# Performance work log

Measured on AMD Instinct MI355X. Metric: run time of the kernel, lower is better.

The kernel has to match this reference:

```python
import jax, jax.numpy as jnp
import numpy as np

B, H, W = 16, 16, 16
DIM = 768
NH = 8
HD = DIM // NH
NEXP = 8
TOPK = 2
DSTATE = 1
DTRANK = 4
KDIR = 4


def setup_inputs() -> dict:
    key = jax.random.key(0)
    ks = jax.random.split(key, 16)
    s = 1.0 / float(np.sqrt(DIM))
    inp = {
        'x': jax.random.normal(ks[0], (B, H, W, DIM)),
        'sa_in_w': jax.random.normal(ks[1], (3 * DIM, DIM)) * s,
        'sa_in_b': jnp.zeros((3 * DIM,)),
        'sa_out_w': jax.random.normal(ks[2], (DIM, DIM)) * s,
        'sa_out_b': jnp.zeros((DIM,)),
        'ca_in_w': jax.random.normal(ks[3], (2 * DIM, DIM)) * s,
        'ca_in_b': jnp.zeros((2 * DIM,)),
        'expert_queries': jax.random.normal(ks[4], (NEXP, DIM)) * s,
        'e_in_w': jax.random.normal(ks[5], (NEXP, 2 * DIM, DIM)) * s,
        'e_in_b': jnp.zeros((NEXP, 2 * DIM)),
        'e_conv_w': jax.random.normal(ks[6], (NEXP, DIM, 1, 3, 3)) / 3.0,
        'e_conv_b': jnp.zeros((NEXP, DIM)),
        'e_xproj_w': jax.random.normal(ks[7], (NEXP, KDIR, DTRANK + 2 * DSTATE, DIM)) * s,
        'e_dtproj_w': jax.random.normal(ks[8], (NEXP, KDIR, DIM, DTRANK)) * 0.1,
        'e_dtproj_b': jax.random.uniform(ks[9], (NEXP, KDIR, DIM), minval=-4.0, maxval=-2.0),
        'e_Alog': jax.random.uniform(ks[10], (NEXP, KDIR, DIM, DSTATE), minval=0.0, maxval=1.0),
        'e_D': jnp.ones((NEXP, KDIR, DIM)),
        'e_ln_scale': jnp.ones((NEXP, DIM)),
        'e_ln_bias': jnp.zeros((NEXP, DIM)),
    }
    return {k: v.astype(jnp.float32) for k, v in inp.items()}


def _selective_scan(xs, Wx, Wdt, bdt, Alog, D):
    # xs: [B, L, d]; Wx: [R+2N, d]; Wdt: [d, R]; Alog: [d, N]; D: [d]
    dbl = jnp.einsum('bld,ed->ble', xs, Wx)
    dt = jax.nn.softplus(jnp.einsum('blr,dr->bld', dbl[..., :DTRANK], Wdt) + bdt)
    Bm = dbl[..., DTRANK:DTRANK + DSTATE]
    Cm = dbl[..., DTRANK + DSTATE:]
    A = -jnp.exp(Alog)  # [d, N]

    def step(h, t):
        dt_t, B_t, C_t, x_t = t  # [b,d],[b,N],[b,N],[b,d]
        h = jnp.exp(dt_t[:, :, None] * A) * h + (dt_t * x_t)[:, :, None] * B_t[:, None, :]
        return h, jnp.einsum('bdn,bn->bd', h, C_t)

    b, L, d = xs.shape
    h0 = jnp.zeros((b, d, DSTATE), xs.dtype)
    tm = lambda a: jnp.moveaxis(a, 1, 0)
    _, ys = jax.lax.scan(step, h0, (tm(dt), tm(Bm), tm(Cm), tm(xs)))
    return jnp.moveaxis(ys, 0, 1) + D * xs


def _expert(in_w, in_b, conv_w, conv_b, xproj_w, dtp_w, dtp_b, Alog, D, ln_s, ln_b, x):
    b = x.shape[0]
    xz = jnp.einsum('bhwc,oc->bhwo', x, in_w) + in_b
    xc, z = jnp.split(xz, 2, axis=-1)
    xn = jax.lax.conv_general_dilated(jnp.transpose(xc, (0, 3, 1, 2)), conv_w,
                                      (1, 1), ((1, 1), (1, 1)), feature_group_count=DIM)
    xc = jax.nn.silu(jnp.transpose(xn + conv_b[None, :, None, None], (0, 2, 3, 1)))
    L = H * W
    xh = xc.reshape(b, L, DIM)                              # row-major 'h'
    xv = jnp.transpose(xc, (0, 2, 1, 3)).reshape(b, L, DIM)  # col-major 'v'
    seqs = jnp.stack([xh, xh[:, ::-1], xv, xv[:, ::-1]])     # [4, b, L, d]
    ys = jax.vmap(_selective_scan)(seqs, xproj_w, dtp_w, dtp_b, Alog, D)
    yv = ys[2] + ys[3][:, ::-1]
    yv = jnp.transpose(yv.reshape(b, W, H, DIM), (0, 2, 1, 3)).reshape(b, L, DIM)
    y = (ys[0] + ys[1][:, ::-1] + yv).reshape(b, H, W, DIM)
    mu = y.mean(-1, keepdims=True)
    var = ((y - mu) ** 2).mean(-1, keepdims=True)
    y = (y - mu) * jax.lax.rsqrt(var + 1e-5) * ln_s + ln_b   # out_norm (LayerNorm)
    y = y * jax.nn.silu(z)
    return y.mean((1, 2))  # AdaptiveAvgPool2d((1,1)) -> [b, DIM]


def _forward(x, sa_in_w, sa_in_b, sa_out_w, sa_out_b, ca_in_w, ca_in_b, expert_queries,
             e_in_w, e_in_b, e_conv_w, e_conv_b, e_xproj_w, e_dtproj_w, e_dtproj_b,
             e_Alog, e_D, e_ln_scale, e_ln_bias):
    b = x.shape[0]
    L = H * W
    scale = 1.0 / float(np.sqrt(HD))
    xs = x.reshape(b, L, DIM)
    # spatial self-attention (eval mode: dropout off)
    qkv = xs @ sa_in_w.T + sa_in_b
    q, k, v = [a.reshape(b, L, NH, HD) for a in jnp.split(qkv, 3, -1)]
    att = jax.nn.softmax(jnp.einsum('bqhd,bkhd->bhqk', q, k) * scale, -1)
    ctx = jnp.einsum('bhqk,bkhd->bqhd', att, v).reshape(b, L, DIM) @ sa_out_w.T + sa_out_b
    # expert cross-attention: only head-averaged attention weights are used
    q2 = (ctx @ ca_in_w[:DIM].T + ca_in_b[:DIM]).reshape(b, L, NH, HD)
    k2 = (expert_queries @ ca_in_w[DIM:].T + ca_in_b[DIM:]).reshape(NEXP, NH, HD)
    aw = jax.nn.softmax(jnp.einsum('blhd,ehd->bhle', q2, k2) * scale, -1).mean(1)  # [b,L,E]
    gate = jax.nn.softmax(aw.mean(1), -1)  # [b, E]
    tk_scores, tk_idx = jax.lax.top_k(gate, TOPK)
    wgt = jax.nn.softmax(tk_scores, -1)
    # dense expert compute (all experts on all samples), then gather top-k
    all_out = jax.vmap(_expert, in_axes=(0,) * 11 + (None,))(
        e_in_w, e_in_b, e_conv_w, e_conv_b, e_xproj_w, e_dtproj_w, e_dtproj_b,
        e_Alog, e_D, e_ln_scale, e_ln_bias, x)  # [E, b, DIM]
    per_b = jnp.transpose(all_out, (1, 0, 2))  # [b, E, DIM]
    sel = jnp.take_along_axis(per_b, tk_idx[:, :, None], axis=1)  # [b, K, DIM]
    return jnp.sum(wgt[:, :, None] * sel, axis=1)  # [b, DIM]


def reference(x, sa_in_w, sa_in_b, sa_out_w, sa_out_b, ca_in_w, ca_in_b, expert_queries,
              e_in_w, e_in_b, e_conv_w, e_conv_b, e_xproj_w, e_dtproj_w, e_dtproj_b,
              e_Alog, e_D, e_ln_scale, e_ln_bias):
    return _forward(x, sa_in_w, sa_in_b, sa_out_w, sa_out_b, ca_in_w, ca_in_b, expert_queries,
                    e_in_w, e_in_b, e_conv_w, e_conv_b, e_xproj_w, e_dtproj_w, e_dtproj_b,
                    e_Alog, e_D, e_ln_scale, e_ln_bias)
```

## Files before the change

kernel.cpp:

```cpp
#include <hip/hip_runtime.h>
#include <hip/hip_bf16.h>


#define LTOK 256
#define DIMC 768

typedef unsigned short ushortt;
typedef __attribute__((ext_vector_type(8))) short bf16x8;
typedef __attribute__((ext_vector_type(4))) float f32x4;

#define LOG2E 1.44269504f
#define LN2   0.69314718f

__device__ __forceinline__ float fexp2(float x) { return __builtin_amdgcn_exp2f(x); }
__device__ __forceinline__ float flog2(float x) { return __builtin_amdgcn_logf(x); }

__device__ __forceinline__ ushortt f2b(float f) {
  union { float f; unsigned u; } c; c.f = f;
  unsigned r = (c.u + 0x7FFFu + ((c.u >> 16) & 1u)) >> 16;
  return (ushortt)r;
}

__global__ __launch_bounds__(256) void mk_mcast4(
    const float* __restrict__ s0, ushortt* __restrict__ d0,
    const float* __restrict__ s1, ushortt* __restrict__ d1,
    const float* __restrict__ s2, ushortt* __restrict__ d2,
    const float* __restrict__ s3, ushortt* __restrict__ d3)
{
  long g = (long)blockIdx.x * 256 + threadIdx.x;
  const float* s; ushortt* dst; long o;
  if (g < 786432)       { s = s0; dst = d0; o = g; }
  else if (g < 1228800) { s = s1; dst = d1; o = g - 786432; }
  else if (g < 1376256) { s = s2; dst = d2; o = g - 1228800; }
  else                  { s = s3; dst = d3; o = g - 1376256; }
  o <<= 2;
  float4 v = *(const float4*)(s + o);
  ushort4 w;
  w.x = f2b(v.x); w.y = f2b(v.y); w.z = f2b(v.z); w.w = f2b(v.w);
  *(ushort4*)(dst + o) = w;
}

__global__ __launch_bounds__(256) void mk_cast(const float* __restrict__ in,
                                               ushortt* __restrict__ outp, long n)
{
  long i = ((long)blockIdx.x * 256 + threadIdx.x) * 4;
  if (i + 3 < n) {
    float4 v = *(const float4*)(in + i);
    ushort4 o;
    o.x = f2b(v.x); o.y = f2b(v.y); o.z = f2b(v.z); o.w = f2b(v.w);
    *(ushort4*)(outp + i) = o;
  }
}

__global__ __launch_bounds__(256) void mk_mfma(
    const ushortt* __restrict__ A, const ushortt* __restrict__ B,
    const float* __restrict__ bias, void* __restrict__ C,
    int K, int lda, int ldb, int ldc,
    int zdiv, long sA1, long sA2, long sB1, long sB2, long sC1, long sC2,
    long sBias,
    const int* __restrict__ pairExp, int tilesN,
    int outBf, int splitN, void* __restrict__ C2, int ldc2, int outBf2, int c2vt)
{
  int z = blockIdx.y;
  long aoff, boff, coff, biasoff = 0;
  if (pairExp) {
    int e = pairExp[z];
    aoff = (long)(z >> 1) * sA1; boff = (long)e * sB1;
    coff = (long)z * sC1; biasoff = (long)e * sBias;
  } else {
    int z1 = z / zdiv, z2 = z - z1 * zdiv;
    aoff = (long)z1 * sA1 + (long)z2 * sA2;
    boff = (long)z1 * sB1 + (long)z2 * sB2;
    coff = (long)z1 * sC1 + (long)z2 * sC2;
  }
  int tile = blockIdx.x;
  int tm = tile / tilesN, tn = tile - tm * tilesN;
  long m0 = (long)tm << 7, n0 = (long)tn << 7;

  __shared__ ushortt As[128][40];
  __shared__ ushortt Bs[128][40];

  int tid = threadIdx.x;
  int lane = tid & 63, wvi = tid >> 6;
  int wr = wvi >> 1, wc = wvi & 1;
  int lm = lane & 15, lg = lane >> 4;

  f32x4 zero4 = {0.f, 0.f, 0.f, 0.f};
  f32x4 acc[4][4];
#pragma unroll
  for (int i = 0; i < 4; i++)
#pragma unroll
    for (int j = 0; j < 4; j++) acc[i][j] = zero4;

  const ushortt* Ab = A + aoff;
  const ushortt* Bb = B + boff;

  for (int k0 = 0; k0 < K; k0 += 32) {
#pragma unroll
    for (int h = 0; h < 2; h++) {
      int q = tid + h * 256;
      int row = q >> 2, ck = (q & 3) << 3;
      *(uint4*)&As[row][ck] = *(const uint4*)(Ab + (m0 + row) * lda + k0 + ck);
      *(uint4*)&Bs[row][ck] = *(const uint4*)(Bb + (n0 + row) * ldb + k0 + ck);
    }
    __syncthreads();
    bf16x8 af[4], bfr[4];
#pragma unroll
    for (int i = 0; i < 4; i++)
      af[i] = *(const bf16x8*)&As[wr * 64 + i * 16 + lm][lg << 3];
#pragma unroll
    for (int j = 0; j < 4; j++)
      bfr[j] = *(const bf16x8*)&Bs[wc * 64 + j * 16 + lm][lg << 3];
#pragma unroll
    for (int i = 0; i < 4; i++)
#pragma unroll
      for (int j = 0; j < 4; j++)
        acc[i][j] = __builtin_amdgcn_mfma_f32_16x16x32_bf16(af[i], bfr[j], acc[i][j], 0, 0, 0);
    __syncthreads();
  }

#pragma unroll
  for (int mt = 0; mt < 4; mt++) {
#pragma unroll
    for (int nt = 0; nt < 4; nt++) {
      long grow = m0 + wr * 64 + mt * 16 + lg * 4;
      long gcol = n0 + wc * 64 + nt * 16 + lm;
      float bv = bias ? bias[biasoff + gcol] : 0.f;
      if ((int)gcol < splitN) {
#pragma unroll
        for (int r = 0; r < 4; r++) {
          float v = acc[mt][nt][r] + bv;
          long idx = coff + (grow + r) * ldc + gcol;
          if (outBf) ((ushortt*)C)[idx] = f2b(v);
          else ((float*)C)[idx] = v;
        }
      } else if (c2vt) {
        int cc = (int)gcol - splitN;
        int hh = cc / 96, jj = cc - hh * 96;
#pragma unroll
        for (int r = 0; r < 4; r++) {
          float v = acc[mt][nt][r] + bv;
          long gr = grow + r;
          long b = gr >> 8, t = gr & 255;
          long idx = (((b * 8 + hh) * 128 + jj) << 8) + t;
          ((ushortt*)C2)[idx] = f2b(v);
        }
      } else {
        long col = gcol - splitN;
#pragma unroll
        for (int r = 0; r < 4; r++) {
          float v = acc[mt][nt][r] + bv;
          long idx = coff + (grow + r) * ldc2 + col;
          if (outBf2) ((ushortt*)C2)[idx] = f2b(v);
          else ((float*)C2)[idx] = v;
        }
      }
    }
  }
}

__global__ __launch_bounds__(256) void mk_gemm(
    const float* __restrict__ A, const float* __restrict__ B,
    const float* __restrict__ bias, float* __restrict__ C,
    int M, int N, int K, int lda, int ldb, int ldc, int tilesN)
{
  int tile = blockIdx.x;
  int tm = tile / tilesN, tn = tile - tm * tilesN;
  int m0 = tm << 6, n0 = tn << 6;

  __shared__ float As[16][68];
  __shared__ float Bs[16][68];

  int tid = threadIdx.x;
  int tx = tid & 15, ty = tid >> 4;
  int lrow = tid >> 2;
  int lk = (tid & 3) << 2;

  float acc[4][4];
#pragma unroll
  for (int i = 0; i < 4; i++)
#pragma unroll
    for (int j = 0; j < 4; j++) acc[i][j] = 0.f;

  for (int k0 = 0; k0 < K; k0 += 16) {
    {
      int gm = m0 + lrow;
      float4 v = {0.f, 0.f, 0.f, 0.f};
      if (gm < M) v = *(const float4*)(A + (long)gm * lda + (k0 + lk));
      As[lk + 0][lrow] = v.x; As[lk + 1][lrow] = v.y;
      As[lk + 2][lrow] = v.z; As[lk + 3][lrow] = v.w;
    }
    {
      int gn = n0 + lrow;
      float4 v = {0.f, 0.f, 0.f, 0.f};
      if (gn < N) v = *(const float4*)(B + (long)gn * ldb + (k0 + lk));
      Bs[lk + 0][lrow] = v.x; Bs[lk + 1][lrow] = v.y;
      Bs[lk + 2][lrow] = v.z; Bs[lk + 3][lrow] = v.w;
    }
    __syncthreads();
#pragma unroll
    for (int kk = 0; kk < 16; kk++) {
      float4 a = *(const float4*)&As[kk][ty << 2];
      float4 b = *(const float4*)&Bs[kk][tx << 2];
      acc[0][0] += a.x * b.x; acc[0][1] += a.x * b.y; acc[0][2] += a.x * b.z; acc[0][3] += a.x * b.w;
      acc[1][0] += a.y * b.x; acc[1][1] += a.y * b.y; acc[1][2] += a.y * b.z; acc[1][3] += a.y * b.w;
      acc[2][0] += a.z * b.x; acc[2][1] += a.z * b.y; acc[2][2] += a.z * b.z; acc[2][3] += a.z * b.w;
      acc[3][0] += a.w * b.x; acc[3][1] += a.w * b.y; acc[3][2] += a.w * b.z; acc[3][3] += a.w * b.w;
    }
    __syncthreads();
  }

#pragma unroll
  for (int i = 0; i < 4; i++) {
    int gm = m0 + (ty << 2) + i;
    if (gm >= M) continue;
#pragma unroll
    for (int j = 0; j < 4; j++) {
      int gn = n0 + (tx << 2) + j;
      if (gn >= N) continue;
      float v = acc[i][j];
      if (bias) v += bias[gn];
      C[(long)gm * ldc + gn] = v;
    }
  }
}

__global__ __launch_bounds__(256) void mk_softmax(const float* __restrict__ scores,
                                                  ushortt* __restrict__ att, float scale)
{
  int row = (blockIdx.x << 2) + (threadIdx.x >> 6);
  int lane = threadIdx.x & 63;
  const float* p = scores + (long)row * 256 + (lane << 2);
  float4 v = *(const float4*)p;
  float m = fmaxf(fmaxf(v.x, v.y), fmaxf(v.z, v.w));
#pragma unroll
  for (int o = 32; o; o >>= 1) m = fmaxf(m, __shfl_xor(m, o, 64));
  float sl = scale * LOG2E;
  v.x = fexp2(sl * (v.x - m));
  v.y = fexp2(sl * (v.y - m));
  v.z = fexp2(sl * (v.z - m));
  v.w = fexp2(sl * (v.w - m));
  float s = v.x + v.y + v.z + v.w;
#pragma unroll
  for (int o = 32; o; o >>= 1) s += __shfl_xor(s, o, 64);
  float r = 1.f / s;
  ushort4 o4;
  o4.x = f2b(v.x * r); o4.y = f2b(v.y * r); o4.z = f2b(v.z * r); o4.w = f2b(v.w * r);
  *(ushort4*)(att + (long)row * 256 + (lane << 2)) = o4;
}

__global__ __launch_bounds__(256) void mk_gates(const float* __restrict__ q2,
                                                const float* __restrict__ k2,
                                                float* __restrict__ gacc)
{
  __shared__ float k2p[8 * 808];
  int b = blockIdx.x >> 4, q = blockIdx.x & 15;
  for (int i = threadIdx.x; i < 6144; i += 256) {
    int e = i / 768, rem = i - e * 768;
    int h = rem / 96, j = rem - h * 96;
    k2p[e * 808 + h * 100 + j] = k2[i];
  }
  __syncthreads();
  const float scale = 0.10206207261596577f;
  int wid = threadIdx.x >> 6, lane = threadIdx.x & 63;
  int h = lane >> 3, e = lane & 7;
  const float* kp = &k2p[e * 808 + h * 100];
  float accL = 0.f;
#pragma unroll
  for (int ti = 0; ti < 4; ti++) {
    int l = q * 16 + wid * 4 + ti;
    const float* qh = q2 + ((long)b * LTOK + l) * DIMC + h * 96;
    float sum = 0.f;
#pragma unroll
    for (int j = 0; j < 96; j += 4) {
      float4 qv = *(const float4*)(qh + j);
      float4 kv = *(const float4*)(kp + j);
      sum += qv.x * kv.x + qv.y * kv.y + qv.z * kv.z + qv.w * kv.w;
    }
    float s = sum * scale;
    float mx = s;
#pragma unroll
    for (int o = 1; o <= 4; o <<= 1) mx = fmaxf(mx, __shfl_xor(mx, o, 64));
    float ex = fexp2((s - mx) * LOG2E);
    float se = ex;
#pragma unroll
    for (int o = 1; o <= 4; o <<= 1) se += __shfl_xor(se, o, 64);
    accL += ex / se;
  }
#pragma unroll
  for (int o = 8; o <= 32; o <<= 1) accL += __shfl_xor(accL, o, 64);
  __shared__ float red[4][8];
  if (lane < 8) red[wid][lane] = accL;
  __syncthreads();
  if (threadIdx.x < 8) {
    float v = red[0][threadIdx.x] + red[1][threadIdx.x] +
              red[2][threadIdx.x] + red[3][threadIdx.x];
    atomicAdd(&gacc[b * 8 + threadIdx.x], v);
  }
}

__global__ __launch_bounds__(64) void mk_gatetop(const float* __restrict__ gacc,
                                                 int* __restrict__ pe,
                                                 float* __restrict__ pw)
{
  int b = threadIdx.x;
  if (b >= 16) return;
  float g[8];
  for (int e = 0; e < 8; e++) g[e] = gacc[b * 8 + e] * (1.f / (8.f * 256.f));
  float mx = g[0];
  for (int e = 1; e < 8; e++) mx = fmaxf(mx, g[e]);
  float se = 0.f;
  for (int e = 0; e < 8; e++) { g[e] = expf(g[e] - mx); se += g[e]; }
  for (int e = 0; e < 8; e++) g[e] /= se;
  int i0 = 0;
  for (int e = 1; e < 8; e++) if (g[e] > g[i0]) i0 = e;
  int i1 = (i0 == 0) ? 1 : 0;
  for (int e = 0; e < 8; e++) if (e != i0 && g[e] > g[i1]) i1 = e;
  float w0 = 1.f / (1.f + expf(g[i1] - g[i0]));
  pe[2 * b] = i0; pe[2 * b + 1] = i1;
  pw[2 * b] = w0; pw[2 * b + 1] = 1.f - w0;
}

__global__ __launch_bounds__(768) void mk_conv(const float* __restrict__ xzx,
                                               const float* __restrict__ cw,
                                               const float* __restrict__ cb,
                                               const int* __restrict__ pe,
                                               float* __restrict__ xc)
{
  int blk = blockIdx.x;
  int p = blk >> 8, t = blk & 255;
  int e = pe[p];
  int h = t >> 4, w = t & 15;
  int c = threadIdx.x;
  const float* wp = cw + ((long)e * DIMC + c) * 9;
  float acc = cb[e * DIMC + c];
#pragma unroll
  for (int dh = 0; dh < 3; dh++) {
    int hh = h + dh - 1;
    if (hh < 0 || hh > 15) continue;
#pragma unroll
    for (int dw = 0; dw < 3; dw++) {
      int ww = w + dw - 1;
      if (ww < 0 || ww > 15) continue;
      acc += xzx[((long)p * LTOK + hh * 16 + ww) * DIMC + c] * wp[dh * 3 + dw];
    }
  }
  xc[((long)p * LTOK + t) * DIMC + c] = acc / (1.f + fexp2(-acc * LOG2E));
}

__device__ __forceinline__ int tmap(int dir, int s) {
  if (dir == 0) return s;
  if (dir == 1) return 255 - s;
  if (dir == 2) return ((s & 15) << 4) | (s >> 4);
  int u = 255 - s;
  return ((u & 15) << 4) | (u >> 4);
}

__global__ __launch_bounds__(256) void mk_dbl(const float* __restrict__ xc,
                                              const float* __restrict__ xproj,
                                              const int* __restrict__ pe,
                                              float* __restrict__ dblm)
{
  int p = blockIdx.x >> 6;
  int tq = blockIdx.x & 63;
  int wid = threadIdx.x >> 6, lane = threadIdx.x & 63;
  int m = tq * 4 + wid;
  int e = pe[p];
  const float* xr = xc + ((long)p * LTOK + m) * DIMC;
  const float* wb = xproj + (long)e * 24 * DIMC;
  float4 xv[3];
#pragma unroll
  for (int j = 0; j < 3; j++) xv[j] = *(const float4*)(xr + j * 256 + lane * 4);
  float acc[24];
#pragma unroll
  for (int r = 0; r < 24; r++) {
    const float* wr = wb + r * DIMC;
    float s = 0.f;
#pragma unroll
    for (int j = 0; j < 3; j++) {
      float4 wv = *(const float4*)(wr + j * 256 + lane * 4);
      s += xv[j].x * wv.x + xv[j].y * wv.y + xv[j].z * wv.z + xv[j].w * wv.w;
    }
    acc[r] = s;
  }
#pragma unroll
  for (int r = 0; r < 24; r++)
#pragma unroll
    for (int o = 32; o; o >>= 1) acc[r] += __shfl_xor(acc[r], o, 64);
  if (lane == 0) {
    float* o = dblm + ((long)p * LTOK + m) * 24;
#pragma unroll
    for (int r = 0; r < 24; r++) o[r] = acc[r];
  }
}

__global__ __launch_bounds__(512) void mk_scan(const float* __restrict__ xc,
                                               const float* __restrict__ dblm,
                                               const float* __restrict__ dtw,
                                               const float* __restrict__ dtb,
                                               const float* __restrict__ Alog,
                                               const float* __restrict__ Dp,
                                               const int* __restrict__ pe,
                                               float* __restrict__ yac)
{
  __shared__ float dbS[256 * 24];
  __shared__ float yS[256 * 17];
  __shared__ float aS[32][16];
  __shared__ float hS[32][16];
  __shared__ float dsum[16];
  int blk = blockIdx.x;
  int p = blk / 48, cg = blk - p * 48;
  int c0 = cg << 4;
  int e = pe[p];
  int tid = threadIdx.x;
  {
    const float4* src = (const float4*)(dblm + (long)p * LTOK * 24);
    float4* dst = (float4*)dbS;
    for (int i = tid; i < 1536; i += 512) dst[i] = src[i];
  }
  for (int i = tid; i < 256 * 17; i += 512) yS[i] = 0.f;
  if (tid < 16) {
    float s = 0.f;
#pragma unroll
    for (int dd = 0; dd < 4; dd++) s += Dp[(long)(e * 4 + dd) * DIMC + c0 + tid];
    dsum[tid] = s;
  }
  __syncthreads();

  int c = tid & 15;
  int rr = tid >> 4;
  int seg = rr & 7;
  int dir = rr >> 3;
  int d = c0 + c;
  const float* xcp = xc + (long)p * LTOK * DIMC;
  long pb = (long)(e * 4 + dir) * DIMC + d;
  float4 wv = *(const float4*)(dtw + pb * 4);
  float bdt = dtb[pb];
  float Ad = -fexp2(Alog[pb] * LOG2E);
  int t0 = seg << 5;

  float h = 0.f, ap = 1.f;
  for (int tb = 0; tb < 32; tb += 8) {
    float xv[8]; int mm[8];
#pragma unroll
    for (int i = 0; i < 8; i++) {
      mm[i] = tmap(dir, t0 + tb + i);
      xv[i] = xcp[(long)mm[i] * DIMC + d];
    }
#pragma unroll
    for (int i = 0; i < 8; i++) {
      const float* db = &dbS[mm[i] * 24 + dir * 6];
      float xr = wv.x * db[0] + wv.y * db[1] + wv.z * db[2] + wv.w * db[3] + bdt;
      float te = fexp2(xr * LOG2E);
      float g = flog2(1.f + te);
      g = (xr > 60.f) ? xr * LOG2E : g;
      float de = fexp2(g * Ad);
      h = de * h + (g * LN2) * xv[i] * db[4];
      ap *= de;
    }
  }
  aS[rr][c] = ap;
  hS[rr][c] = h;
  __syncthreads();

  float hh = 0.f;
  for (int j = dir * 8; j < rr; j++)
    hh = aS[j][c] * hh + hS[j][c];

  for (int tb = 0; tb < 32; tb += 8) {
    float xv[8]; int mm[8];
#pragma unroll
    for (int i = 0; i < 8; i++) {
      mm[i] = tmap(dir, t0 + tb + i);
      xv[i] = xcp[(long)mm[i] * DIMC + d];
    }
#pragma unroll
    for (int i = 0; i < 8; i++) {
      const float* db = &dbS[mm[i] * 24 + dir * 6];
      float xr = wv.x * db[0] + wv.y * db[1] + wv.z * db[2] + wv.w * db[3] + bdt;
      float te = fexp2(xr * LOG2E);
      float g = flog2(1.f + te);
      g = (xr > 60.f) ? xr * LOG2E : g;
      float de = fexp2(g * Ad);
      hh = de * hh + (g * LN2) * xv[i] * db[4];
      atomicAdd(&yS[mm[i] * 17 + c], hh * db[5]);
    }
  }
  __syncthreads();

  float* yp = yac + (long)p * LTOK * DIMC + c0;
  for (int i = tid; i < 256 * 16; i += 512) {
    int t = i >> 4, cz = i & 15;
    yp[(long)t * DIMC + cz] = yS[t * 17 + cz] + xcp[(long)t * DIMC + c0 + cz] * dsum[cz];
  }
}

__global__ __launch_bounds__(256) void mk_lnfin(const float* __restrict__ yac,
                                                const float* __restrict__ xzz,
                                                const float* __restrict__ lns,
                                                const float* __restrict__ lnb,
                                                const int* __restrict__ pe,
                                                float* __restrict__ eo)
{
  int blk = blockIdx.x;
  int p = blk >> 4, ts = blk & 15;
  int e = pe[p];
  int tid = threadIdx.x;
  int wid = tid >> 6, lane = tid & 63;
  float ls[12], lb[12], acc[12];
#pragma unroll
  for (int i = 0; i < 12; i++) {
    int d = i * 64 + lane;
    ls[i] = lns[e * DIMC + d];
    lb[i] = lnb[e * DIMC + d];
    acc[i] = 0.f;
  }
#pragma unroll
  for (int tt = 0; tt < 4; tt++) {
    int t = ts * 16 + wid * 4 + tt;
    const float* yr = yac + ((long)p * LTOK + t) * DIMC;
    const float* zr = xzz + ((long)p * LTOK + t) * DIMC;
    float v[12];
    float s = 0.f;
#pragma unroll
    for (int i = 0; i < 12; i++) { v[i] = yr[i * 64 + lane]; s += v[i]; }
#pragma unroll
    for (int o = 32; o; o >>= 1) s += __shfl_xor(s, o, 64);
    float mu = s * (1.f / 768.f);
    float sq = 0.f;
#pragma unroll
    for (int i = 0; i < 12; i++) { float dlt = v[i] - mu; sq += dlt * dlt; }
#pragma unroll
    for (int o = 32; o; o >>= 1) sq += __shfl_xor(sq, o, 64);
    float rs = rsqrtf(sq * (1.f / 768.f) + 1e-5f);
#pragma unroll
    for (int i = 0; i < 12; i++) {
      float y = (v[i] - mu) * rs * ls[i] + lb[i];
      float z = zr[i * 64 + lane];
      y *= z / (1.f + fexp2(-z * LOG2E));
      acc[i] += y;
    }
  }
  __shared__ float sacc[768];
  for (int j = tid; j < 768; j += 256) sacc[j] = 0.f;
  __syncthreads();
#pragma unroll
  for (int i = 0; i < 12; i++) atomicAdd(&sacc[i * 64 + lane], acc[i]);
  __syncthreads();
  for (int j = tid; j < 768; j += 256) atomicAdd(&eo[(long)p * DIMC + j], sacc[j]);
}

__global__ __launch_bounds__(768) void mk_out(const float* __restrict__ eo,
                                              const float* __restrict__ pw,
                                              float* __restrict__ out)
{
  int b = blockIdx.x, d = threadIdx.x;
  float v = pw[2 * b] * eo[(long)(2 * b) * DIMC + d] +
            pw[2 * b + 1] * eo[(long)(2 * b + 1) * DIMC + d];
  out[b * DIMC + d] = v * (1.f / 256.f);
}

extern "C" void kernel_launch(void* const* d_in, const int* in_sizes, int n_in,
                              void* d_out, int out_size, void* d_ws, size_t ws_size,
                              hipStream_t stream)
{
  const float* x        = (const float*)d_in[0];
  const float* sa_in_w  = (const float*)d_in[1];
  const float* sa_in_b  = (const float*)d_in[2];
  const float* sa_out_w = (const float*)d_in[3];
  const float* sa_out_b = (const float*)d_in[4];
  const float* ca_in_w  = (const float*)d_in[5];
  const float* ca_in_b  = (const float*)d_in[6];
  const float* eq       = (const float*)d_in[7];
  const float* e_in_w   = (const float*)d_in[8];
  const float* e_in_b   = (const float*)d_in[9];
  const float* e_conv_w = (const float*)d_in[10];
  const float* e_conv_b = (const float*)d_in[11];
  const float* e_xproj  = (const float*)d_in[12];
  const float* e_dtw    = (const float*)d_in[13];
  const float* e_dtb    = (const float*)d_in[14];
  const float* e_Alog   = (const float*)d_in[15];
  const float* e_D      = (const float*)d_in[16];
  const float* e_lns    = (const float*)d_in[17];
  const float* e_lnb    = (const float*)d_in[18];
  float* out = (float*)d_out;

  float* ws = (float*)d_ws;
  ushortt* qk_b   = (ushortt*)(ws + 0);
  float*   scores = ws + 6291456;
  ushortt* dump_b = (ushortt*)(ws + 6291456);
  ushortt* ctxa_b = (ushortt*)(ws + 7864320);
  ushortt* att_b  = (ushortt*)(ws + 14680064);
  ushortt* vt_b   = (ushortt*)(ws + 18874368);
  ushortt* xb     = (ushortt*)(ws + 20971520);
  ushortt* wqkv_b = (ushortt*)(ws + 22544384);
  ushortt* saow_b = (ushortt*)(ws + 23429120);
  ushortt* caw_b  = (ushortt*)(ws + 23724032);
  ushortt* ctx_b  = (ushortt*)(ws + 0);
  float*   q2     = ws + 1572864;
  float*   k2     = ws + 25165824;
  int*     pe     = (int*)(ws + 25171968);
  float*   pw     = ws + 25172000;
  float*   eo     = ws + 25172032;
  float*   dblm   = ws + 25196608;
  float*   gacc   = ws + 25393216;
  float*   xz_x   = ws + 0;
  float*   xz_z   = ws + 6291456;
  ushortt* ew_b   = (ushortt*)(ws + 12582912);
  float*   xc     = ws + 12582912;
  float*   yac    = ws + 18874368;

  const float scale = 0.10206207261596577f;

  mk_mcast4<<<5952, 256, 0, stream>>>(x, xb, sa_in_w, wqkv_b, sa_out_w, saow_b,
                                      ca_in_w, caw_b);
  mk_mfma<<<dim3(576, 1), 256, 0, stream>>>(xb, wqkv_b, sa_in_b, qk_b,
      768, 768, 768, 1536, 1, 0, 0, 0, 0, 0, 0, 0, nullptr, 18,
      1, 1536, vt_b, 0, 1, 1);
  mk_mfma<<<dim3(4, 128), 256, 0, stream>>>(qk_b, qk_b + 768, nullptr, scores,
      96, 1536, 1536, 256, 8, 393216, 96, 393216, 96, 524288, 65536, 0, nullptr, 2,
      0, 1 << 30, nullptr, 0, 0, 0);
  mk_softmax<<<8192, 256, 0, stream>>>(scores, att_b, scale);
  mk_mfma<<<dim3(2, 128), 256, 0, stream>>>(att_b, vt_b, nullptr, ctxa_b,
      256, 256, 256, 768, 8, 524288, 65536, 262144, 32768, 196608, 96, 0, nullptr, 1,
      1, 96, dump_b, 32, 1, 0);
  mk_cast<<<9216, 256, 0, stream>>>(e_in_w, ew_b, 9437184);
  mk_mfma<<<dim3(192, 1), 256, 0, stream>>>(ctxa_b, saow_b, sa_out_b, ctx_b,
      768, 768, 768, 768, 1, 0, 0, 0, 0, 0, 0, 0, nullptr, 6,
      1, 1 << 30, nullptr, 0, 0, 0);
  mk_mfma<<<dim3(192, 1), 256, 0, stream>>>(ctx_b, caw_b, ca_in_b, q2,
      768, 768, 768, 768, 1, 0, 0, 0, 0, 0, 0, 0, nullptr, 6,
      0, 1 << 30, nullptr, 0, 0, 0);
  mk_gemm<<<dim3(12, 1), 256, 0, stream>>>(eq, ca_in_w + 589824, ca_in_b + 768, k2,
      8, 768, 768, 768, 768, 768, 12);
  (void)hipMemsetAsync(gacc, 0, 128 * sizeof(float), stream);
  (void)hipMemsetAsync(eo, 0, 24576 * sizeof(float), stream);
  mk_gates<<<256, 256, 0, stream>>>(q2, k2, gacc);
  mk_gatetop<<<1, 64, 0, stream>>>(gacc, pe, pw);
  mk_mfma<<<dim3(24, 32), 256, 0, stream>>>(xb, ew_b, e_in_b, xz_x,
      768, 768, 768, 768, 1, 196608, 0, 1179648, 0, 196608, 0, 1536, pe, 12,
      0, 768, xz_z, 768, 0, 0);
  mk_conv<<<32 * 256, 768, 0, stream>>>(xz_x, e_conv_w, e_conv_b, pe, xc);
  mk_dbl<<<2048, 256, 0, stream>>>(xc, e_xproj, pe, dblm);
  mk_scan<<<1536, 512, 0, stream>>>(xc, dblm, e_dtw, e_dtb, e_Alog, e_D, pe, yac);
  mk_lnfin<<<512, 256, 0, stream>>>(yac, xz_z, e_lns, e_lnb, pe, eo);
  mk_out<<<16, 768, 0, stream>>>(eo, pw, out);

  (void)in_sizes; (void)n_in; (void)out_size; (void)ws_size;
}
```

Baseline: 635.0 us.

## Stage scan inputs in LDS with swizzled layouts and cache first-pass decay terms

The selective-scan kernel now copies its xc tile into shared memory once, with a padded and swizzled layout, instead of reading global memory in both scan passes. The dblm buffer is padded to 32 floats per token so the dt/B/C values can be fetched as float4 loads with a bank-rotating swizzle. The first pass keeps per-step decay and increment values in registers so the second pass skips recomputing the exp/log softplus. The change also adds an occupancy hint to launch bounds and moves dblm to workspace offset 0, which raises register pressure and risks spills or aliasing with live buffers.

```diff
diff --git a/kernel.cpp b/kernel.cpp
--- a/kernel.cpp
+++ b/kernel.cpp
@@ -388,13 +388,13 @@
 #pragma unroll
     for (int o = 32; o; o >>= 1) acc[r] += __shfl_xor(acc[r], o, 64);
   if (lane == 0) {
-    float* o = dblm + ((long)p * LTOK + m) * 24;
-#pragma unroll
-    for (int r = 0; r < 24; r++) o[r] = acc[r];
-  }
-}
-
-__global__ __launch_bounds__(512) void mk_scan(const float* __restrict__ xc,
+    float* o = dblm + ((long)p * LTOK + m) * 32;
+#pragma unroll
+    for (int r = 0; r < 24; r++) o[(r / 6) * 8 + (r - (r / 6) * 6)] = acc[r];
+  }
+}
+
+__global__ __launch_bounds__(512, 4) void mk_scan(const float* __restrict__ xc,
                                                const float* __restrict__ dblm,
                                                const float* __restrict__ dtw,
                                                const float* __restrict__ dtb,
@@ -403,10 +403,10 @@
                                                const int* __restrict__ pe,
                                                float* __restrict__ yac)
 {
-  __shared__ float dbS[256 * 24];
+  __shared__ __attribute__((aligned(16))) float dbS[256 * 36];
   __shared__ float yS[256 * 17];
-  __shared__ float aS[32][16];
-  __shared__ float hS[32][16];
+  __shared__ __attribute__((aligned(16))) float xS[256 * 20];
+  __shared__ float ahS[32][16][2];
   __shared__ float dsum[16];
   int blk = blockIdx.x;
   int p = blk / 48, cg = blk - p * 48;
@@ -414,9 +414,20 @@
   int e = pe[p];
   int tid = threadIdx.x;
   {
-    const float4* src = (const float4*)(dblm + (long)p * LTOK * 24);
-    float4* dst = (float4*)dbS;
-    for (int i = tid; i < 1536; i += 512) dst[i] = src[i];
+    const float4* src = (const float4*)(dblm + (long)p * LTOK * 32);
+    for (int i = tid; i < 2048; i += 512) {
+      int t = i >> 3, c4 = i & 7;
+      int rot = (t >> 5) & 7;
+      *(float4*)&dbS[t * 36 + (((c4 + rot) & 7) << 2)] = src[i];
+    }
+  }
+  {
+    const float* xcp = xc + (long)p * LTOK * DIMC + c0;
+    for (int i = tid; i < 1024; i += 512) {
+      int t = i >> 2, c4 = i & 3;
+      *(float4*)&xS[t * 20 + (((t >> 5) & 1) << 2) + (c4 << 2)] =
+          *(const float4*)(xcp + (long)t * DIMC + (c4 << 2));
+    }
   }
   for (int i = tid; i < 256 * 17; i += 512) yS[i] = 0.f;
   if (tid < 16) {
@@ -432,66 +443,73 @@
   int seg = rr & 7;
   int dir = rr >> 3;
   int d = c0 + c;
-  const float* xcp = xc + (long)p * LTOK * DIMC;
   long pb = (long)(e * 4 + dir) * DIMC + d;
   float4 wv = *(const float4*)(dtw + pb * 4);
   float bdt = dtb[pb];
   float Ad = -fexp2(Alog[pb] * LOG2E);
   int t0 = seg << 5;
-
+  int stp = (dir == 0) ? 1 : (dir == 1) ? -1 : (dir == 2) ? 16 : -16;
+
+  float de[32], inc[32];
   float h = 0.f, ap = 1.f;
+#pragma unroll
   for (int tb = 0; tb < 32; tb += 8) {
-    float xv[8]; int mm[8];
+    int mb = tmap(dir, t0 + tb);
 #pragma unroll
     for (int i = 0; i < 8; i++) {
-      mm[i] = tmap(dir, t0 + tb + i);
-      xv[i] = xcp[(long)mm[i] * DIMC + d];
-    }
+      int mm = mb + i * stp;
+      int rot = (mm >> 5) & 7;
+      float4 dv = *(const float4*)&dbS[mm * 36 + (((dir * 2 + rot) & 7) << 2)];
+      float Bv = dbS[mm * 36 + (((dir * 2 + 1 + rot) & 7) << 2)];
+      float xl = (wv.x * dv.x + wv.y * dv.y + wv.z * dv.z + wv.w * dv.w + bdt) * LOG2E;
+      float te = fexp2(xl);
+      float g = flog2(1.f + te);
+      g = (xl > 86.f) ? xl : g;
+      float dei = fexp2(g * Ad);
+      float xsv = xS[mm * 20 + (((mm >> 5) & 1) << 2) + c];
+      float inci = (g * LN2) * xsv * Bv;
+      de[tb + i] = dei; inc[tb + i] = inci;
+      h = dei * h + inci;
+      ap *= dei;
+    }
+  }
+  ahS[rr][c][0] = ap;
+  ahS[rr][c][1] = h;
+  __syncthreads();
+
+  float hh = 0.f;
+  {
+    int base = dir << 3;
+    float av[8], hv[8];
+#pragma unroll
+    for (int j = 0; j < 8; j++) {
+      av[j] = ahS[base + j][c][0];
+      hv[j] = ahS[base + j][c][1];
+    }
+#pragma unroll
+    for (int j = 0; j < 7; j++)
+      if (j < seg) hh = av[j] * hh + hv[j];
+  }
+
+#pragma unroll
+  for (int tb = 0; tb < 32; tb += 8) {
+    int mb = tmap(dir, t0 + tb);
 #pragma unroll
     for (int i = 0; i < 8; i++) {
-      const float* db = &dbS[mm[i] * 24 + dir * 6];
-      float xr = wv.x * db[0] + wv.y * db[1] + wv.z * db[2] + wv.w * db[3] + bdt;
-      float te = fexp2(xr * LOG2E);
-      float g = flog2(1.f + te);
-      g = (xr > 60.f) ? xr * LOG2E : g;
-      float de = fexp2(g * Ad);
-      h = de * h + (g * LN2) * xv[i] * db[4];
-      ap *= de;
-    }
-  }
-  aS[rr][c] = ap;
-  hS[rr][c] = h;
+      int mm = mb + i * stp;
+      int rot = (mm >> 5) & 7;
+      float cv = dbS[mm * 36 + (((dir * 2 + 1 + rot) & 7) << 2) + 1];
+      hh = de[tb + i] * hh + inc[tb + i];
+      atomicAdd(&yS[mm * 17 + c], hh * cv);
+    }
+  }
   __syncthreads();
 
-  float hh = 0.f;
-  for (int j = dir * 8; j < rr; j++)
-    hh = aS[j][c] * hh + hS[j][c];
-
-  for (int tb = 0; tb < 32; tb += 8) {
-    float xv[8]; int mm[8];
-#pragma unroll
-    for (int i = 0; i < 8; i++) {
-      mm[i] = tmap(dir, t0 + tb + i);
-      xv[i] = xcp[(long)mm[i] * DIMC + d];
-    }
-#pragma unroll
-    for (int i = 0; i < 8; i++) {
-      const float* db = &dbS[mm[i] * 24 + dir * 6];
-      float xr = wv.x * db[0] + wv.y * db[1] + wv.z * db[2] + wv.w * db[3] + bdt;
-      float te = fexp2(xr * LOG2E);
-      float g = flog2(1.f + te);
-      g = (xr > 60.f) ? xr * LOG2E : g;
-      float de = fexp2(g * Ad);
-      hh = de * hh + (g * LN2) * xv[i] * db[4];
-      atomicAdd(&yS[mm[i] * 17 + c], hh * db[5]);
-    }
-  }
-  __syncthreads();
-
   float* yp = yac + (long)p * LTOK * DIMC + c0;
-  for (int i = tid; i < 256 * 16; i += 512) {
+  for (int i = tid; i < 4096; i += 512) {
     int t = i >> 4, cz = i & 15;
-    yp[(long)t * DIMC + cz] = yS[t * 17 + cz] + xcp[(long)t * DIMC + c0 + cz] * dsum[cz];
+    yp[(long)t * DIMC + cz] = yS[t * 17 + cz] +
+        xS[t * 20 + (((t >> 5) & 1) << 2) + cz] * dsum[cz];
   }
 }
 
@@ -602,13 +620,13 @@
   int*     pe     = (int*)(ws + 25171968);
   float*   pw     = ws + 25172000;
   float*   eo     = ws + 25172032;
-  float*   dblm   = ws + 25196608;
   float*   gacc   = ws + 25393216;
   float*   xz_x   = ws + 0;
   float*   xz_z   = ws + 6291456;
   ushortt* ew_b   = (ushortt*)(ws + 12582912);
   float*   xc     = ws + 12582912;
   float*   yac    = ws + 18874368;
+  float*   dblm   = ws + 0;
 
   const float scale = 0.10206207261596577f;
 
```

Result: slower. 667.3 us (+5.1%).
